# Kernel optimization log

Measured on AMD Instinct MI355X. Metric: run time of the kernel, lower is better.

The kernel has to match this reference:

```python
import jax, jax.numpy as jnp
import numpy as np

B, N, K = 4, 4096, 20
IN_C, OUT_C = 32, 32
EPS = 1e-5


def setup_inputs() -> dict:
    key = jax.random.key(0)
    ks = jax.random.split(key, 10)
    s = 0.05
    return {
        "x": jax.random.normal(ks[0], (B, 3, N), dtype=jnp.float32),
        "feature": jax.random.normal(ks[1], (B, IN_C, N), dtype=jnp.float32),
        "w_mlp": jax.random.normal(ks[2], (IN_C, 7), dtype=jnp.float32) * s,     # Conv1d(7, in_c, 1)
        "b_mlp": jax.random.normal(ks[3], (IN_C,), dtype=jnp.float32) * s,
        "w_att": jax.random.normal(ks[4], (2 * IN_C, 2 * IN_C), dtype=jnp.float32) * s,  # Conv1d(2C,2C,1,bias=False)
        "w_conv": jax.random.normal(ks[5], (OUT_C, 2 * IN_C), dtype=jnp.float32) * s,    # Linear(2C,out_c)
        "b_conv": jax.random.normal(ks[6], (OUT_C,), dtype=jnp.float32) * s,
        "w_out": jax.random.normal(ks[7], (OUT_C, IN_C), dtype=jnp.float32) * s,  # Conv1d(in_c,out_c,1)
        "b_out": jax.random.normal(ks[8], (OUT_C,), dtype=jnp.float32) * s,
        "gamma": jnp.ones((OUT_C,), dtype=jnp.float32),   # BatchNorm1d weight
        "beta": jnp.zeros((OUT_C,), dtype=jnp.float32),   # BatchNorm1d bias
    }


def reference(x, feature, w_mlp, b_mlp, w_att, w_conv, b_conv, w_out, b_out, gamma, beta):
    pts = jnp.swapaxes(x, 1, 2)                       # [B, N, 3]
    # brute-force KNN (argkmin over squared distance); self is nearest (d=0)
    sq = jnp.sum(pts * pts, axis=-1)                  # [B, N]
    d2 = sq[:, :, None] + sq[:, None, :] - 2.0 * jnp.einsum('bnd,bmd->bnm', pts, pts)
    neigh = jax.lax.top_k(-d2, K)[1]                  # [B, N, K] int32

    gather = jax.vmap(lambda v, idx: v[idx])          # per-batch fancy gather
    x_neighs = gather(pts, neigh)                     # [B, N, K, 3]
    x_repeat = jnp.broadcast_to(x_neighs[:, :, 0:1, :], x_neighs.shape)
    x_rel = x_neighs - x_repeat                       # [B, N, K, 3]
    x_dis = jnp.linalg.norm(x_rel, axis=-1, keepdims=True)  # [B, N, K, 1]
    x_feats = jnp.concatenate([x_repeat, x_rel, x_dis], axis=-1)   # [B, N, K, 7]
    x_enc = jnp.einsum('bnkf,cf->bnkc', x_feats, w_mlp) + b_mlp    # [B, N, K, C]

    feat_pts = jnp.swapaxes(feature, 1, 2)            # [B, N, C]
    feat_neighs = gather(feat_pts, neigh)             # [B, N, K, C]
    feats = jnp.concatenate([feat_neighs, x_enc], axis=-1)         # [B, N, K, 2C]

    # attention weights: pointwise conv then softmax over the CHANNEL dim (torch dim=1)
    scores = jnp.einsum('bnkc,dc->bnkd', feats, w_att)             # [B, N, K, 2C]
    attn = jax.nn.softmax(scores, axis=-1)
    pooled = jnp.sum(attn * feats, axis=2)            # sum over neighbors K -> [B, N, 2C]

    out_feat = jnp.einsum('bnc,oc->bno', pooled, w_conv) + b_conv  # [B, N, out_c]
    out_feat = jnp.swapaxes(out_feat, 1, 2)           # [B, out_c, N]
    out_feat = out_feat + jnp.einsum('oc,bcn->bon', w_out, feature) + b_out[None, :, None]

    # BatchNorm1d (training-mode batch statistics over B and N)
    mean = jnp.mean(out_feat, axis=(0, 2), keepdims=True)
    var = jnp.var(out_feat, axis=(0, 2), keepdims=True)
    normed = (out_feat - mean) * jax.lax.rsqrt(var + EPS)
    return normed * gamma[None, :, None] + beta[None, :, None]
```

## Files before the change

### kernel.cpp

```cpp
#include <hip/hip_runtime.h>
#include <hip/hip_bf16.h>

#define BATCH 4
#define NPTS  4096
#define KNBR  20
#define INC   32
#define TWC   64
#define OUTC  32
#define EPSBN 1e-5f

typedef short short8 __attribute__((ext_vector_type(8)));
typedef float f32x16 __attribute__((ext_vector_type(16)));

__device__ __forceinline__ float rlf(float v, int l) {
    return __uint_as_float((unsigned)__builtin_amdgcn_readlane((int)__float_as_uint(v), l));
}
__device__ __forceinline__ ushort f2bf(float x) {
    unsigned u = __float_as_uint(x);
    unsigned r = u + 0x7FFFu + ((u >> 16) & 1u);
    return (ushort)(r >> 16);
}
__device__ __forceinline__ float bf2f(ushort h) {
    return __uint_as_float(((unsigned)h) << 16);
}
__device__ __forceinline__ void gll16(const float4* g, float4* l) {
    __builtin_amdgcn_global_load_lds((const __attribute__((address_space(1))) void*)g,
                                     (__attribute__((address_space(3))) void*)l, 16, 0, 0);
}

__global__ __launch_bounds__(256) void k_prep(const float* __restrict__ x,
                                              const float* __restrict__ f,
                                              float4* __restrict__ xT4,
                                              ushort* __restrict__ fT,
                                              const float* __restrict__ w_att,
                                              const float* __restrict__ w_conv,
                                              const float* __restrict__ w_out,
                                              const float* __restrict__ w_mlp,
                                              const float* __restrict__ b_mlp,
                                              short8* __restrict__ wattF,
                                              short8* __restrict__ wconvF,
                                              short8* __restrict__ woutF,
                                              float* __restrict__ wmlp8) {
    int i = blockIdx.x * 256 + threadIdx.x;
    if (i < BATCH * NPTS) {
        int b = i / NPTS, n = i % NPTS;
        const float* xb = x + (size_t)b * 3 * NPTS;
        float x0 = xb[n], x1 = xb[NPTS + n], x2 = xb[2 * NPTS + n];
        float sq = fmaf(x2, x2, fmaf(x1, x1, x0 * x0));
        xT4[i] = make_float4(x0, x1, x2, sq);
    }
    if (i < BATCH * INC * NPTS) {
        int n = i % NPTS; int t = i / NPTS; int c = t % INC; int b = t / INC;
        fT[((size_t)(b * NPTS + n)) * INC + c] = f2bf(f[i]);
    }
    if (blockIdx.x == gridDim.x - 1) {
        int t = threadIdx.x;
        for (int idx = t; idx < 14 * 64; idx += 256) {
            int fr = idx >> 6, ln = idx & 63, l31 = ln & 31, h8 = (ln >> 5) * 8;
            short8 v;
            if (fr < 8) {
                int nt = fr >> 2, kt = fr & 3;
                const float* s = w_att + (nt * 32 + l31) * 64 + kt * 16 + h8;
#pragma unroll
                for (int j = 0; j < 8; ++j) v[j] = (short)f2bf(s[j]);
                wattF[fr * 64 + ln] = v;
            } else if (fr < 12) {
                int kt = fr - 8;
                const float* s = w_conv + l31 * 64 + kt * 16 + h8;
#pragma unroll
                for (int j = 0; j < 8; ++j) v[j] = (short)f2bf(s[j]);
                wconvF[kt * 64 + ln] = v;
            } else {
                int kt = fr - 12;
                const float* s = w_out + l31 * 32 + kt * 16 + h8;
#pragma unroll
                for (int j = 0; j < 8; ++j) v[j] = (short)f2bf(s[j]);
                woutF[kt * 64 + ln] = v;
            }
        }
        for (int idx = t; idx < 512; idx += 256) {
            int e = idx >> 3, j = idx & 7;
            wmlp8[idx] = (j < 7) ? w_mlp[e * 7 + j] : b_mlp[e];
        }
    }
}

#define CAP   256
#define PPBK  8
__global__ __launch_bounds__(512, 6) void k_fused(const float4* __restrict__ xT4,
                                                  const ushort* __restrict__ fbT,
                                                  const float* __restrict__ wmlp8,
                                                  const short8* __restrict__ wattF,
                                                  const short8* __restrict__ wconvF,
                                                  const short8* __restrict__ woutF,
                                                  float* __restrict__ out) {
    __shared__ __align__(16) char smA[32768];
    float4*             candB = (float4*)smA;
    unsigned long long* survB = (unsigned long long*)(smA + 16384);
    ushort*             FbB   = (ushort*)smA;
    __shared__ int scnt[PPBK], slot[PPBK];
    __shared__ int neighL[PPBK][KNBR];
    __shared__ __align__(16) ushort pool[PPBK][64];

    const int tid  = threadIdx.x;
    const int lane = tid & 63;
    const int wv   = tid >> 6;
    const int hi   = lane >> 5;
    const int l31  = lane & 31;
    const int gp   = blockIdx.x * PPBK + wv;
    const int b    = gp >> 12;
    const int nb   = gp & (NPTS - 1);
    const float4* base = xT4 + (size_t)b * NPTS;

    if (lane == 0) { scnt[wv] = 0; slot[wv] = 1; }

    float4 me = xT4[gp];

    auto stage = [&](int c) {
        const float4* src = base + c * 512 + wv * 64 + lane;
        float4* dst = candB + (c & 1) * 512 + wv * 64;
        gll16(src, dst);
    };

    stage(0); stage(1);
    __syncthreads();

    unsigned bits[16];
    unsigned lmin = 0xFFFFFFFFu, lmin2 = 0xFFFFFFFFu;
#pragma unroll
    for (int j = 0; j < 8; ++j) {
        float4 o = candB[lane + 64 * j];
        float dot = fmaf(o.z, me.z, fmaf(o.y, me.y, o.x * me.x));
        unsigned bb = __float_as_uint(fmaxf((me.w + o.w) - 2.0f * dot, 0.0f));
        bits[j] = bb;
        unsigned lo_ = bb < lmin ? bb : lmin;
        unsigned hi_ = bb < lmin ? lmin : bb;
        lmin = lo_;
        lmin2 = hi_ < lmin2 ? hi_ : lmin2;
    }
#pragma unroll
    for (int j = 0; j < 8; ++j) {
        float4 o = candB[512 + lane + 64 * j];
        float dot = fmaf(o.z, me.z, fmaf(o.y, me.y, o.x * me.x));
        unsigned bb = __float_as_uint(fmaxf((me.w + o.w) - 2.0f * dot, 0.0f));
        bits[8 + j] = bb;
        unsigned lo_ = bb < lmin ? bb : lmin;
        unsigned hi_ = bb < lmin ? lmin : bb;
        lmin = lo_;
        lmin2 = hi_ < lmin2 ? hi_ : lmin2;
    }
    __syncthreads();
    stage(2);

    unsigned lo = 0u, hi2 = 0xFF000000u;
    for (int it = 0; it < 16 && lo < hi2; ++it) {
        unsigned mid = lo + ((hi2 - lo) >> 1);
        int c = __popcll(__ballot(lmin <= mid)) + __popcll(__ballot(lmin2 <= mid));
        if (c >= KNBR) hi2 = mid; else lo = mid + 1;
    }
    const unsigned tau = hi2;

#pragma unroll
    for (int j = 0; j < 16; ++j) {
        if (bits[j] <= tau) {
            int pos = atomicAdd(&scnt[wv], 1);
            if (pos < CAP)
                survB[wv * CAP + pos] = ((unsigned long long)bits[j] << 32) | (unsigned)(lane + 64 * j);
        }
    }
    __syncthreads();

    for (int ch = 2; ch < 8; ++ch) {
        if (ch < 7) stage(ch + 1);
        const float4* cb = candB + (ch & 1) * 512;
        const int ib = ch * 512 + lane;
#pragma unroll
        for (int j = 0; j < 8; ++j) {
            float4 o = cb[lane + 64 * j];
            float dot = fmaf(o.z, me.z, fmaf(o.y, me.y, o.x * me.x));
            unsigned bb = __float_as_uint(fmaxf((me.w + o.w) - 2.0f * dot, 0.0f));
            if (bb <= tau) {
                int pos = atomicAdd(&scnt[wv], 1);
                if (pos < CAP)
                    survB[wv * CAP + pos] = ((unsigned long long)bb << 32) | (unsigned)(ib + 64 * j);
            }
        }
        __syncthreads();
    }

    int cnt = scnt[wv]; if (cnt > CAP) cnt = CAP;
    const unsigned long long* sv = survB + wv * CAP;

    if (cnt <= 128) {
        unsigned long long k0 = (lane      < cnt) ? sv[lane     ] : ~0ull;
        unsigned long long k1 = (lane + 64 < cnt) ? sv[lane + 64] : ~0ull;
        unsigned d0 = (unsigned)(k0 >> 32), d1 = (unsigned)(k1 >> 32);
        unsigned i0 = (unsigned)k0, i1 = (unsigned)k1;

        unsigned th;
        {
            unsigned l2 = 0u, h2 = tau;
            bool found = false;
            for (int it = 0; it < 32; ++it) {
                unsigned mid = l2 + ((h2 - l2) >> 1);
                int c = __popcll(__ballot(d0 <= mid)) + __popcll(__ballot(d1 <= mid));
                if (c >= KNBR) h2 = mid; else l2 = mid + 1;
                if (c == KNBR) {
                    unsigned mm = (d0 <= mid) ? d0 : 0u;
                    unsigned m2_ = (d1 <= mid) ? d1 : 0u;
                    mm = mm > m2_ ? mm : m2_;
#pragma unroll
                    for (int off = 32; off >= 1; off >>= 1) {
                        unsigned o = __shfl_xor(mm, off, 64);
                        mm = o > mm ? o : mm;
                    }
                    th = mm; found = true; break;
                }
                if (l2 >= h2) break;
            }
            if (!found) th = h2;
        }
        int cless = __popcll(__ballot(d0 < th)) + __popcll(__ballot(d1 < th));
        int need = KNBR - cless;
        bool t0 = (d0 == th), t1 = (d1 == th);
        int tcnt = __popcll(__ballot(t0)) + __popcll(__ballot(t1));
        unsigned idxthr = 0xFFFFFFFFu;
        if (tcnt != need) {
            unsigned la = 0u, ha = 0xFFFFFFFFu;
            for (int it = 0; it < 32; ++it) {
                unsigned mid = la + ((ha - la) >> 1);
                int c = __popcll(__ballot(t0 && i0 <= mid)) + __popcll(__ballot(t1 && i1 <= mid));
                if (c >= need) ha = mid; else la = mid + 1;
            }
            idxthr = ha;
        }
        bool s0 = (d0 < th) || (t0 && i0 <= idxthr);
        bool s1 = (d1 < th) || (t1 && i1 <= idxthr);

        unsigned long long mk = k0 < k1 ? k0 : k1;
#pragma unroll
        for (int off = 32; off >= 1; off >>= 1) {
            unsigned long long o = __shfl_xor(mk, off, 64);
            mk = o < mk ? o : mk;
        }
        if (s0) { if (k0 == mk) neighL[wv][0] = (int)i0; else { int p = atomicAdd(&slot[wv], 1); neighL[wv][p] = (int)i0; } }
        if (s1) { if (k1 == mk) neighL[wv][0] = (int)i1; else { int p = atomicAdd(&slot[wv], 1); neighL[wv][p] = (int)i1; } }
    } else {
        unsigned long long k0 = (lane       < cnt) ? sv[lane      ] : ~0ull;
        unsigned long long k1 = (lane +  64 < cnt) ? sv[lane +  64] : ~0ull;
        unsigned long long k2 = (lane + 128 < cnt) ? sv[lane + 128] : ~0ull;
        unsigned long long k3 = (lane + 192 < cnt) ? sv[lane + 192] : ~0ull;
        unsigned d0 = (unsigned)(k0 >> 32), d1 = (unsigned)(k1 >> 32);
        unsigned d2 = (unsigned)(k2 >> 32), d3 = (unsigned)(k3 >> 32);
        unsigned i0 = (unsigned)k0, i1 = (unsigned)k1, i2 = (unsigned)k2, i3 = (unsigned)k3;

        unsigned l2 = 0u, h2 = tau;
        for (int it = 0; it < 32 && l2 < h2; ++it) {
            unsigned mid = l2 + ((h2 - l2) >> 1);
            int c = __popcll(__ballot(d0 <= mid)) + __popcll(__ballot(d1 <= mid))
                  + __popcll(__ballot(d2 <= mid)) + __popcll(__ballot(d3 <= mid));
            if (c >= KNBR) h2 = mid; else l2 = mid + 1;
        }
        const unsigned th = h2;
        int cless = __popcll(__ballot(d0 < th)) + __popcll(__ballot(d1 < th))
                  + __popcll(__ballot(d2 < th)) + __popcll(__ballot(d3 < th));
        int need = KNBR - cless;
        bool t0 = (d0 == th), t1 = (d1 == th), t2 = (d2 == th), t3 = (d3 == th);
        int tcnt = __popcll(__ballot(t0)) + __popcll(__ballot(t1))
                 + __popcll(__ballot(t2)) + __popcll(__ballot(t3));
        unsigned idxthr = 0xFFFFFFFFu;
        if (tcnt != need) {
            unsigned la = 0u, ha = 0xFFFFFFFFu;
            for (int it = 0; it < 32; ++it) {
                unsigned mid = la + ((ha - la) >> 1);
                int c = __popcll(__ballot(t0 && i0 <= mid)) + __popcll(__ballot(t1 && i1 <= mid))
                      + __popcll(__ballot(t2 && i2 <= mid)) + __popcll(__ballot(t3 && i3 <= mid));
                if (c >= need) ha = mid; else la = mid + 1;
            }
            idxthr = ha;
        }
        bool s0 = (d0 < th) || (t0 && i0 <= idxthr);
        bool s1 = (d1 < th) || (t1 && i1 <= idxthr);
        bool s2 = (d2 < th) || (t2 && i2 <= idxthr);
        bool s3 = (d3 < th) || (t3 && i3 <= idxthr);

        unsigned long long m01 = k0 < k1 ? k0 : k1;
        unsigned long long m23 = k2 < k3 ? k2 : k3;
        unsigned long long mk  = m01 < m23 ? m01 : m23;
#pragma unroll
        for (int off = 32; off >= 1; off >>= 1) {
            unsigned long long o = __shfl_xor(mk, off, 64);
            mk = o < mk ? o : mk;
        }
        if (s0) { if (k0 == mk) neighL[wv][0] = (int)i0; else { int p = atomicAdd(&slot[wv], 1); neighL[wv][p] = (int)i0; } }
        if (s1) { if (k1 == mk) neighL[wv][0] = (int)i1; else { int p = atomicAdd(&slot[wv], 1); neighL[wv][p] = (int)i1; } }
        if (s2) { if (k2 == mk) neighL[wv][0] = (int)i2; else { int p = atomicAdd(&slot[wv], 1); neighL[wv][p] = (int)i2; } }
        if (s3) { if (k3 == mk) neighL[wv][0] = (int)i3; else { int p = atomicAdd(&slot[wv], 1); neighL[wv][p] = (int)i3; } }
    }

    __syncthreads();

    const ushort* fb = fbT + (size_t)b * NPTS * INC;
    ushort* Fw = FbB + wv * 2048;

    int nv = 0;
    if (l31 < KNBR) nv = neighL[wv][l31];
    float4 ncl = base[nv];

    float wm[8];
    {
        const float4* w8 = (const float4*)(wmlp8 + l31 * 8);
        float4 a = w8[0], bq = w8[1];
        wm[0] = a.x; wm[1] = a.y; wm[2] = a.z; wm[3] = a.w;
        wm[4] = bq.x; wm[5] = bq.y; wm[6] = bq.z; wm[7] = bq.w;
    }
    const float c0x = rlf(ncl.x, 0), c0y = rlf(ncl.y, 0), c0z = rlf(ncl.z, 0);

    ushort fr[KNBR];
#pragma unroll
    for (int k = 0; k < KNBR; ++k) {
        int snk = __builtin_amdgcn_readlane(nv, k);
        fr[k] = fb[(size_t)snk * INC + l31];
    }

    float fmbase = wm[7];
    fmbase = fmaf(wm[0], c0x, fmbase); fmbase = fmaf(wm[1], c0y, fmbase);
    fmbase = fmaf(wm[2], c0z, fmbase);
#pragma unroll
    for (int k = 0; k < KNBR; ++k) {
        float rx = rlf(ncl.x, k) - c0x;
        float ry = rlf(ncl.y, k) - c0y;
        float rz = rlf(ncl.z, k) - c0z;
        float dis = sqrtf(fmaf(rz, rz, fmaf(ry, ry, rx * rx)));
        float fm = fmbase;
        fm = fmaf(wm[3], rx, fm);  fm = fmaf(wm[4], ry, fm);  fm = fmaf(wm[5], rz, fm);
        fm = fmaf(wm[6], dis, fm);
        ushort fbits = hi ? f2bf(fm) : fr[k];
        Fw[k * 64 + (lane ^ ((k & 7) << 3))] = fbits;
    }

    short8 Af[4];
#pragma unroll
    for (int kt = 0; kt < 4; ++kt) {
        int c0 = kt * 16 + 8 * hi;
        Af[kt] = *(const short8*)&Fw[l31 * 64 + (c0 ^ ((l31 & 7) << 3))];
    }

    float mloc, zloc;
    {
        f32x16 af;
#pragma unroll
        for (int i = 0; i < 16; ++i) af[i] = 0.f;
        __builtin_amdgcn_s_setprio(1);
#pragma unroll
        for (int kt = 0; kt < 4; ++kt)
            af = __builtin_amdgcn_mfma_f32_32x32x16_bf16(wattF[kt * 64 + lane], Af[kt], af, 0, 0, 0);
        __builtin_amdgcn_s_setprio(0);
        float m0 = af[0];
#pragma unroll
        for (int i = 1; i < 16; ++i) m0 = fmaxf(m0, af[i]);
        float z0 = 0.f;
#pragma unroll
        for (int i = 0; i < 16; ++i) z0 += __expf(af[i] - m0);
        mloc = m0; zloc = z0;
    }
    {
        f32x16 af;
#pragma unroll
        for (int i = 0; i < 16; ++i) af[i] = 0.f;
        __builtin_amdgcn_s_setprio(1);
#pragma unroll
        for (int kt = 0; kt < 4; ++kt)
            af = __builtin_amdgcn_mfma_f32_32x32x16_bf16(wattF[(4 + kt) * 64 + lane], Af[kt], af, 0, 0, 0);
        __builtin_amdgcn_s_setprio(0);
        float m1 = af[0];
#pragma unroll
        for (int i = 1; i < 16; ++i) m1 = fmaxf(m1, af[i]);
        float z1 = 0.f;
#pragma unroll
        for (int i = 0; i < 16; ++i) z1 += __expf(af[i] - m1);
        float mn = fmaxf(mloc, m1);
        zloc = zloc * __expf(mloc - mn) + z1 * __expf(m1 - mn);
        mloc = mn;
    }
    float mo = fmaxf(mloc, __shfl_xor(mloc, 32, 64));
    float zs = zloc * __expf(mloc - mo);
    float Zk = zs + __shfl_xor(zs, 32, 64);
    float invZ = 1.0f / Zk;

    float pooled0 = 0.f, pooled1 = 0.f;
    {
        f32x16 acc;
#pragma unroll
        for (int i = 0; i < 16; ++i) acc[i] = 0.f;
        __builtin_amdgcn_s_setprio(1);
#pragma unroll
        for (int kt = 0; kt < 4; ++kt)
            acc = __builtin_amdgcn_mfma_f32_32x32x16_bf16(Af[kt], wattF[kt * 64 + lane], acc, 0, 0, 0);
        __builtin_amdgcn_s_setprio(0);
#pragma unroll
        for (int r = 0; r < 12; ++r) {
            int j = (r & 3) + 8 * (r >> 2) + 4 * hi;
            float mzm = rlf(mo, j);
            float mzi = rlf(invZ, j);
            float a0 = __expf(acc[r] - mzm) * mzi;
            float f0 = bf2f(Fw[j * 64 + (l31 ^ ((j & 7) << 3))]);
            float p0 = a0 * f0;
            if (r >= 8) p0 = hi ? 0.f : p0;
            pooled0 += p0;
        }
    }
    {
        f32x16 acc;
#pragma unroll
        for (int i = 0; i < 16; ++i) acc[i] = 0.f;
        __builtin_amdgcn_s_setprio(1);
#pragma unroll
        for (int kt = 0; kt < 4; ++kt)
            acc = __builtin_amdgcn_mfma_f32_32x32x16_bf16(Af[kt], wattF[(4 + kt) * 64 + lane], acc, 0, 0, 0);
        __builtin_amdgcn_s_setprio(0);
#pragma unroll
        for (int r = 0; r < 12; ++r) {
            int j = (r & 3) + 8 * (r >> 2) + 4 * hi;
            float mzm = rlf(mo, j);
            float mzi = rlf(invZ, j);
            float a1 = __expf(acc[r] - mzm) * mzi;
            float f1 = bf2f(Fw[j * 64 + ((32 + l31) ^ ((j & 7) << 3))]);
            float p1 = a1 * f1;
            if (r >= 8) p1 = hi ? 0.f : p1;
            pooled1 += p1;
        }
    }
    pooled0 += __shfl_xor(pooled0, 32, 64);
    pooled1 += __shfl_xor(pooled1, 32, 64);
    if (!hi) {
        pool[wv][l31]      = f2bf(pooled0);
        pool[wv][32 + l31] = f2bf(pooled1);
    }

    f32x16 oa;
#pragma unroll
    for (int i = 0; i < 16; ++i) oa[i] = 0.f;
    __builtin_amdgcn_s_setprio(1);
#pragma unroll
    for (int kt = 0; kt < 4; ++kt) {
        short8 bb = *(const short8*)&pool[wv][kt * 16 + 8 * hi];
        oa = __builtin_amdgcn_mfma_f32_32x32x16_bf16(wconvF[kt * 64 + lane], bb, oa, 0, 0, 0);
    }
#pragma unroll
    for (int kt = 0; kt < 2; ++kt) {
        short8 bb = *(const short8*)(fb + (size_t)nb * INC + kt * 16 + 8 * hi);
        oa = __builtin_amdgcn_mfma_f32_32x32x16_bf16(woutF[kt * 64 + lane], bb, oa, 0, 0, 0);
    }
    __builtin_amdgcn_s_setprio(0);
#pragma unroll
    for (int r = 0; r < 16; ++r) {
        int o = (r & 3) + 8 * (r >> 2) + 4 * hi;
        if (l31 == 0) out[((size_t)(b * OUTC + o)) * NPTS + nb] = oa[r];
    }
}

__global__ __launch_bounds__(256) void k_bn(float* __restrict__ of,
                                            const float* __restrict__ gamma,
                                            const float* __restrict__ beta) {
    const int c = blockIdx.x;
    const int tid = threadIdx.x;
    float s = 0.f, s2 = 0.f;
#pragma unroll
    for (int b = 0; b < BATCH; ++b) {
        const float4* p = (const float4*)(of + ((size_t)b * OUTC + c) * NPTS);
        for (int i = tid; i < NPTS / 4; i += 256) {
            float4 v = p[i];
            s += (v.x + v.y) + (v.z + v.w);
            s2 = fmaf(v.x, v.x, s2); s2 = fmaf(v.y, v.y, s2);
            s2 = fmaf(v.z, v.z, s2); s2 = fmaf(v.w, v.w, s2);
        }
    }
#pragma unroll
    for (int off = 32; off >= 1; off >>= 1) {
        s += __shfl_xor(s, off, 64);
        s2 += __shfl_xor(s2, off, 64);
    }
    __shared__ float rs[4], rs2[4];
    __shared__ float sc[2];
    if ((tid & 63) == 0) { rs[tid >> 6] = s; rs2[tid >> 6] = s2; }
    __syncthreads();
    if (tid == 0) {
        float S = (rs[0] + rs[1]) + (rs[2] + rs[3]);
        float S2 = (rs2[0] + rs2[1]) + (rs2[2] + rs2[3]);
        const float invn = 1.0f / (BATCH * NPTS);
        float mean = S * invn;
        float var = S2 * invn - mean * mean;
        float rstd = rsqrtf(var + EPSBN);
        float scale = rstd * gamma[c];
        sc[0] = scale;
        sc[1] = beta[c] - mean * scale;
    }
    __syncthreads();
    const float scale = sc[0], shift = sc[1];
#pragma unroll
    for (int b = 0; b < BATCH; ++b) {
        float4* p = (float4*)(of + ((size_t)b * OUTC + c) * NPTS);
        for (int i = tid; i < NPTS / 4; i += 256) {
            float4 v = p[i];
            v.x = fmaf(v.x, scale, shift);
            v.y = fmaf(v.y, scale, shift);
            v.z = fmaf(v.z, scale, shift);
            v.w = fmaf(v.w, scale, shift);
            p[i] = v;
        }
    }
}

extern "C" void kernel_launch(void* const* d_in, const int* in_sizes, int n_in,
                              void* d_out, int out_size, void* d_ws, size_t ws_size,
                              hipStream_t stream) {
    const float* x      = (const float*)d_in[0];
    const float* feat   = (const float*)d_in[1];
    const float* w_mlp  = (const float*)d_in[2];
    const float* b_mlp  = (const float*)d_in[3];
    const float* w_att  = (const float*)d_in[4];
    const float* w_conv = (const float*)d_in[5];
    const float* w_out  = (const float*)d_in[7];
    const float* gamma  = (const float*)d_in[9];
    const float* beta   = (const float*)d_in[10];
    float* out = (float*)d_out;

    char* ws = (char*)d_ws;
    float4* xT4    = (float4*)ws;
    ushort* fbT    = (ushort*)(ws + 262144);
    short8* wattF  = (short8*)(ws + 1310976);
    short8* wconvF = (short8*)(ws + 1319168);
    short8* woutF  = (short8*)(ws + 1323264);
    float*  wmlp8  = (float*)(ws + 1325312);

    k_prep<<<(BATCH * INC * NPTS + 255) / 256 + 1, 256, 0, stream>>>(
        x, feat, xT4, fbT, w_att, w_conv, w_out, w_mlp, b_mlp,
        wattF, wconvF, woutF, wmlp8);
    k_fused<<<(BATCH * NPTS) / PPBK, 512, 0, stream>>>(xT4, fbT, wmlp8,
                                                       wattF, wconvF, woutF, out);
    k_bn<<<OUTC, 256, 0, stream>>>(out, gamma, beta);
}
```

Measured before the change: 92.00 us.

## Shrink KNN candidate cap and shared tile, compute neighbor geometry per lane

```diff
diff --git a/kernel.cpp b/kernel.cpp
--- a/kernel.cpp
+++ b/kernel.cpp
@@ -85,8 +85,9 @@
     }
 }
 
-#define CAP   256
+#define CAP   192
 #define PPBK  8
+#define FWSZ  (KNBR * 64)
 __global__ __launch_bounds__(512, 6) void k_fused(const float4* __restrict__ xT4,
                                                   const ushort* __restrict__ fbT,
                                                   const float* __restrict__ wmlp8,
@@ -94,7 +95,7 @@
                                                   const short8* __restrict__ wconvF,
                                                   const short8* __restrict__ woutF,
                                                   float* __restrict__ out) {
-    __shared__ __align__(16) char smA[32768];
+    __shared__ __align__(16) char smA[28672];
     float4*             candB = (float4*)smA;
     unsigned long long* survB = (unsigned long long*)(smA + 16384);
     ushort*             FbB   = (ushort*)smA;
@@ -249,32 +250,29 @@
         unsigned long long k0 = (lane       < cnt) ? sv[lane      ] : ~0ull;
         unsigned long long k1 = (lane +  64 < cnt) ? sv[lane +  64] : ~0ull;
         unsigned long long k2 = (lane + 128 < cnt) ? sv[lane + 128] : ~0ull;
-        unsigned long long k3 = (lane + 192 < cnt) ? sv[lane + 192] : ~0ull;
-        unsigned d0 = (unsigned)(k0 >> 32), d1 = (unsigned)(k1 >> 32);
-        unsigned d2 = (unsigned)(k2 >> 32), d3 = (unsigned)(k3 >> 32);
-        unsigned i0 = (unsigned)k0, i1 = (unsigned)k1, i2 = (unsigned)k2, i3 = (unsigned)k3;
+        unsigned d0 = (unsigned)(k0 >> 32), d1 = (unsigned)(k1 >> 32), d2 = (unsigned)(k2 >> 32);
+        unsigned i0 = (unsigned)k0, i1 = (unsigned)k1, i2 = (unsigned)k2;
 
         unsigned l2 = 0u, h2 = tau;
         for (int it = 0; it < 32 && l2 < h2; ++it) {
             unsigned mid = l2 + ((h2 - l2) >> 1);
             int c = __popcll(__ballot(d0 <= mid)) + __popcll(__ballot(d1 <= mid))
-                  + __popcll(__ballot(d2 <= mid)) + __popcll(__ballot(d3 <= mid));
+                  + __popcll(__ballot(d2 <= mid));
             if (c >= KNBR) h2 = mid; else l2 = mid + 1;
         }
         const unsigned th = h2;
         int cless = __popcll(__ballot(d0 < th)) + __popcll(__ballot(d1 < th))
-                  + __popcll(__ballot(d2 < th)) + __popcll(__ballot(d3 < th));
+                  + __popcll(__ballot(d2 < th));
         int need = KNBR - cless;
-        bool t0 = (d0 == th), t1 = (d1 == th), t2 = (d2 == th), t3 = (d3 == th);
-        int tcnt = __popcll(__ballot(t0)) + __popcll(__ballot(t1))
-                 + __popcll(__ballot(t2)) + __popcll(__ballot(t3));
+        bool t0 = (d0 == th), t1 = (d1 == th), t2 = (d2 == th);
+        int tcnt = __popcll(__ballot(t0)) + __popcll(__ballot(t1)) + __popcll(__ballot(t2));
         unsigned idxthr = 0xFFFFFFFFu;
         if (tcnt != need) {
             unsigned la = 0u, ha = 0xFFFFFFFFu;
             for (int it = 0; it < 32; ++it) {
                 unsigned mid = la + ((ha - la) >> 1);
                 int c = __popcll(__ballot(t0 && i0 <= mid)) + __popcll(__ballot(t1 && i1 <= mid))
-                      + __popcll(__ballot(t2 && i2 <= mid)) + __popcll(__ballot(t3 && i3 <= mid));
+                      + __popcll(__ballot(t2 && i2 <= mid));
                 if (c >= need) ha = mid; else la = mid + 1;
             }
             idxthr = ha;
@@ -282,11 +280,9 @@
         bool s0 = (d0 < th) || (t0 && i0 <= idxthr);
         bool s1 = (d1 < th) || (t1 && i1 <= idxthr);
         bool s2 = (d2 < th) || (t2 && i2 <= idxthr);
-        bool s3 = (d3 < th) || (t3 && i3 <= idxthr);
 
         unsigned long long m01 = k0 < k1 ? k0 : k1;
-        unsigned long long m23 = k2 < k3 ? k2 : k3;
-        unsigned long long mk  = m01 < m23 ? m01 : m23;
+        unsigned long long mk  = m01 < k2 ? m01 : k2;
 #pragma unroll
         for (int off = 32; off >= 1; off >>= 1) {
             unsigned long long o = __shfl_xor(mk, off, 64);
@@ -295,13 +291,12 @@
         if (s0) { if (k0 == mk) neighL[wv][0] = (int)i0; else { int p = atomicAdd(&slot[wv], 1); neighL[wv][p] = (int)i0; } }
         if (s1) { if (k1 == mk) neighL[wv][0] = (int)i1; else { int p = atomicAdd(&slot[wv], 1); neighL[wv][p] = (int)i1; } }
         if (s2) { if (k2 == mk) neighL[wv][0] = (int)i2; else { int p = atomicAdd(&slot[wv], 1); neighL[wv][p] = (int)i2; } }
-        if (s3) { if (k3 == mk) neighL[wv][0] = (int)i3; else { int p = atomicAdd(&slot[wv], 1); neighL[wv][p] = (int)i3; } }
     }
 
     __syncthreads();
 
     const ushort* fb = fbT + (size_t)b * NPTS * INC;
-    ushort* Fw = FbB + wv * 2048;
+    ushort* Fw = FbB + wv * FWSZ;
 
     int nv = 0;
     if (l31 < KNBR) nv = neighL[wv][l31];
@@ -323,27 +318,29 @@
         fr[k] = fb[(size_t)snk * INC + l31];
     }
 
+    float rxl = ncl.x - c0x, ryl = ncl.y - c0y, rzl = ncl.z - c0z;
+    float disl = sqrtf(fmaf(rzl, rzl, fmaf(ryl, ryl, rxl * rxl)));
+
     float fmbase = wm[7];
     fmbase = fmaf(wm[0], c0x, fmbase); fmbase = fmaf(wm[1], c0y, fmbase);
     fmbase = fmaf(wm[2], c0z, fmbase);
 #pragma unroll
     for (int k = 0; k < KNBR; ++k) {
-        float rx = rlf(ncl.x, k) - c0x;
-        float ry = rlf(ncl.y, k) - c0y;
-        float rz = rlf(ncl.z, k) - c0z;
-        float dis = sqrtf(fmaf(rz, rz, fmaf(ry, ry, rx * rx)));
         float fm = fmbase;
-        fm = fmaf(wm[3], rx, fm);  fm = fmaf(wm[4], ry, fm);  fm = fmaf(wm[5], rz, fm);
-        fm = fmaf(wm[6], dis, fm);
+        fm = fmaf(wm[3], rlf(rxl, k), fm);
+        fm = fmaf(wm[4], rlf(ryl, k), fm);
+        fm = fmaf(wm[5], rlf(rzl, k), fm);
+        fm = fmaf(wm[6], rlf(disl, k), fm);
         ushort fbits = hi ? f2bf(fm) : fr[k];
         Fw[k * 64 + (lane ^ ((k & 7) << 3))] = fbits;
     }
 
+    const int rowA = (l31 < KNBR) ? l31 : (KNBR - 1);
     short8 Af[4];
 #pragma unroll
     for (int kt = 0; kt < 4; ++kt) {
         int c0 = kt * 16 + 8 * hi;
-        Af[kt] = *(const short8*)&Fw[l31 * 64 + (c0 ^ ((l31 & 7) << 3))];
+        Af[kt] = *(const short8*)&Fw[rowA * 64 + (c0 ^ ((rowA & 7) << 3))];
     }
 
     float mloc, zloc;
@@ -386,7 +383,7 @@
     float mo = fmaxf(mloc, __shfl_xor(mloc, 32, 64));
     float zs = zloc * __expf(mloc - mo);
     float Zk = zs + __shfl_xor(zs, 32, 64);
-    float invZ = 1.0f / Zk;
+    float mzl = mo + __logf(Zk);
 
     float pooled0 = 0.f, pooled1 = 0.f;
     {
@@ -401,9 +398,7 @@
 #pragma unroll
         for (int r = 0; r < 12; ++r) {
             int j = (r & 3) + 8 * (r >> 2) + 4 * hi;
-            float mzm = rlf(mo, j);
-            float mzi = rlf(invZ, j);
-            float a0 = __expf(acc[r] - mzm) * mzi;
+            float a0 = __expf(acc[r] - rlf(mzl, j));
             float f0 = bf2f(Fw[j * 64 + (l31 ^ ((j & 7) << 3))]);
             float p0 = a0 * f0;
             if (r >= 8) p0 = hi ? 0.f : p0;
@@ -422,9 +417,7 @@
 #pragma unroll
         for (int r = 0; r < 12; ++r) {
             int j = (r & 3) + 8 * (r >> 2) + 4 * hi;
-            float mzm = rlf(mo, j);
-            float mzi = rlf(invZ, j);
-            float a1 = __expf(acc[r] - mzm) * mzi;
+            float a1 = __expf(acc[r] - rlf(mzl, j));
             float f1 = bf2f(Fw[j * 64 + ((32 + l31) ^ ((j & 7) << 3))]);
             float p1 = a1 * f1;
             if (r >= 8) p1 = hi ? 0.f : p1;
```

Measured after the change: 84.92 us. 7.7% less time.
